# Optimization experiments

Hardware: AMD Instinct MI355X
Metric: run time of the kernel (lower is better)

## Reference

```python
import jax, jax.numpy as jnp
import numpy as np

D_IN = 2048
H1 = D_IN // 4      # 512
H2 = D_IN // 16     # 128
N_EXP = 8
N_CLS = 10
BATCH = 16384


def setup_inputs() -> dict:
    key = jax.random.key(0)
    ks = jax.random.split(key, 16)
    s = lambda k, shape, fan_in: jax.random.normal(k, shape, jnp.float32) / np.sqrt(fan_in)
    return {
        "fs": jax.random.normal(ks[0], (BATCH, D_IN // 2), jnp.float32),
        "fp": jax.random.normal(ks[1], (BATCH, D_IN // 2), jnp.float32),
        # gate MLP params (output = num_source, softmax)
        "gW1": s(ks[2], (D_IN, H1), D_IN), "gb1": jnp.zeros((H1,), jnp.float32),
        "gW2": s(ks[3], (H1, H2), H1),     "gb2": jnp.zeros((H2,), jnp.float32),
        "gW3": s(ks[4], (H2, N_EXP), H2), "gb3": jnp.zeros((N_EXP,), jnp.float32),
        # stacked expert MLP params (output = num classes, log_softmax)
        "eW1": s(ks[5], (N_EXP, D_IN, H1), D_IN), "eb1": jnp.zeros((N_EXP, H1), jnp.float32),
        "eW2": s(ks[6], (N_EXP, H1, H2), H1),     "eb2": jnp.zeros((N_EXP, H2), jnp.float32),
        "eW3": s(ks[7], (N_EXP, H2, N_CLS), H2),  "eb3": jnp.zeros((N_EXP, N_CLS), jnp.float32),
    }


def reference(fs, fp, gW1, gb1, gW2, gb2, gW3, gb3, eW1, eb1, eW2, eb2, eW3, eb3):
    features = jnp.concatenate([fs, fp], axis=-1)            # [B, D_IN]

    # Gate MLP on detached features (detach is a no-op for fwd), softmax output
    g = jax.nn.relu(features @ gW1 + gb1)
    g = jax.nn.relu(g @ gW2 + gb2)
    gate_outs = jax.nn.softmax(g @ gW3 + gb3, axis=-1)       # [B, E]

    # All experts as batched GEMMs over stacked weights, log_softmax output
    h = jax.nn.relu(jnp.einsum('bd,edh->beh', features, eW1) + eb1[None])   # [B, E, H1]
    h = jax.nn.relu(jnp.einsum('beh,ehk->bek', h, eW2) + eb2[None])         # [B, E, H2]
    logits = jnp.einsum('bek,eko->beo', h, eW3) + eb3[None]                 # [B, E, C]
    expert_outs = jax.nn.log_softmax(logits, axis=-1)                       # [B, E, C]

    # Gate-weighted sum over experts
    output = jnp.einsum('be,bec->bc', gate_outs, expert_outs)               # [B, C]
    return output, gate_outs
```

## Files before the change

### kernel.cpp

```cpp
#include <hip/hip_runtime.h>
#include <hip/hip_bf16.h>

#define B_SZ   16384
#define DIN    2048
#define H1_SZ  512
#define H2_SZ  128
#define N_EXP  8
#define N_CLS  10
#define N1     4608
#define N2     1152

typedef __attribute__((ext_vector_type(8))) __bf16 bf16x8;
typedef __attribute__((ext_vector_type(4))) float  floatx4;
typedef __attribute__((ext_vector_type(4))) short  short4v;
typedef __attribute__((ext_vector_type(8))) short  short8v;

__device__ __forceinline__ float bf2f(short s) {
  unsigned int u = ((unsigned int)(unsigned short)s) << 16;
  float f; __builtin_memcpy(&f, &u, 4); return f;
}

__global__ void convert_features_kernel(const float* __restrict__ fs,
                                        const float* __restrict__ fp,
                                        __hip_bfloat16* __restrict__ X) {
  const int nf8 = B_SZ * (DIN / 8);
  const float4* fs4 = (const float4*)fs;
  const float4* fp4 = (const float4*)fp;
  for (int i = blockIdx.x * blockDim.x + threadIdx.x; i < nf8;
       i += gridDim.x * blockDim.x) {
    int c = i & 255;
    int row = i >> 8;
    float4 v0, v1;
    if (c < 128) {
      v0 = fs4[(size_t)row * 256 + 2 * c];
      v1 = fs4[(size_t)row * 256 + 2 * c + 1];
    } else {
      int cc = c - 128;
      v0 = fp4[(size_t)row * 256 + 2 * cc];
      v1 = fp4[(size_t)row * 256 + 2 * cc + 1];
    }
    union { short8v v8; __hip_bfloat16 h[8]; } u;
    u.h[0] = __float2bfloat16(v0.x);
    u.h[1] = __float2bfloat16(v0.y);
    u.h[2] = __float2bfloat16(v0.z);
    u.h[3] = __float2bfloat16(v0.w);
    u.h[4] = __float2bfloat16(v1.x);
    u.h[5] = __float2bfloat16(v1.y);
    u.h[6] = __float2bfloat16(v1.z);
    u.h[7] = __float2bfloat16(v1.w);
    *(short8v*)(X + (size_t)i * 8) = u.v8;
  }
}

__global__ void transpose_convert_kernel(const float* __restrict__ expert_src,
                                         const float* __restrict__ gate_src,
                                         int K, int H, int E,
                                         __hip_bfloat16* __restrict__ out) {
  __shared__ float t[32][33];
  int k0 = blockIdx.x * 32;
  int n0 = blockIdx.y * 32;
  int e = n0 / H;
  const float* src; int h0;
  if (e < E) { src = expert_src + (size_t)e * K * H; h0 = n0 - e * H; }
  else       { src = gate_src;                       h0 = n0 - E * H; }
  int tx = threadIdx.x, ty = threadIdx.y;
  #pragma unroll
  for (int j = 0; j < 4; ++j) {
    int r = ty + j * 8;
    t[r][tx] = src[(size_t)(k0 + r) * H + h0 + tx];
  }
  __syncthreads();
  #pragma unroll
  for (int j = 0; j < 4; ++j) {
    int r = ty + j * 8;
    out[(size_t)(n0 + r) * K + k0 + tx] = __float2bfloat16(t[tx][r]);
  }
}

template <bool NT>
__device__ __forceinline__ void gemm_core(
    const __hip_bfloat16* __restrict__ A,  int lda,
    const __hip_bfloat16* __restrict__ BT, int K,
    const float* __restrict__ bias,
    __hip_bfloat16* __restrict__ O, int ldo) {
  __shared__ __align__(16) __hip_bfloat16 As[128 * 64];
  __shared__ __align__(16) __hip_bfloat16 Bs[128 * 64];

  const int tid  = threadIdx.x;
  const int lane = tid & 63;
  const int wave = tid >> 6;
  const int wm   = (wave >> 1) * 64;
  const int wn   = (wave & 1) * 64;
  const int lrow  = lane & 15;
  const int lquad = lane >> 4;

  floatx4 acc[4][4] = {};

  for (int k0 = 0; k0 < K; k0 += 64) {
    #pragma unroll
    for (int j = 0; j < 4; ++j) {
      int chunk = j * 256 + tid;
      int mi = chunk >> 3;
      int cs = chunk & 7;
      int cl = cs ^ (mi & 7);
      __builtin_amdgcn_global_load_lds(
          (const __attribute__((address_space(1))) unsigned int*)(A + (size_t)mi * lda + k0 + cl * 8),
          (__attribute__((address_space(3))) unsigned int*)(As + chunk * 8),
          16, 0, 0);
      __builtin_amdgcn_global_load_lds(
          (const __attribute__((address_space(1))) unsigned int*)(BT + (size_t)mi * K + k0 + cl * 8),
          (__attribute__((address_space(3))) unsigned int*)(Bs + chunk * 8),
          16, 0, 0);
    }
    __syncthreads();
    #pragma unroll
    for (int ks = 0; ks < 2; ++ks) {
      bf16x8 a[4], b[4];
      #pragma unroll
      for (int t = 0; t < 4; ++t) {
        int ar = wm + t * 16 + lrow;
        int br = wn + t * 16 + lrow;
        int ca = (ks * 4 + lquad) ^ (ar & 7);
        int cb = (ks * 4 + lquad) ^ (br & 7);
        a[t] = *(const bf16x8*)(As + ar * 64 + ca * 8);
        b[t] = *(const bf16x8*)(Bs + br * 64 + cb * 8);
      }
      #pragma unroll
      for (int mt = 0; mt < 4; ++mt)
        #pragma unroll
        for (int nt = 0; nt < 4; ++nt)
          acc[mt][nt] = __builtin_amdgcn_mfma_f32_16x16x32_bf16(
              a[mt], b[nt], acc[mt][nt], 0, 0, 0);
    }
    __syncthreads();
  }

  #pragma unroll
  for (int nt = 0; nt < 4; ++nt) {
    int col = wn + nt * 16 + lrow;
    float bv = bias[col];
    #pragma unroll
    for (int mt = 0; mt < 4; ++mt) {
      #pragma unroll
      for (int r = 0; r < 4; ++r) {
        int row = wm + mt * 16 + lquad * 4 + r;
        float v = acc[mt][nt][r] + bv;
        v = v > 0.f ? v : 0.f;
        __hip_bfloat16 hv = __float2bfloat16(v);
        if (NT) {
          __builtin_nontemporal_store(
              *reinterpret_cast<unsigned short*>(&hv),
              reinterpret_cast<unsigned short*>(&O[(size_t)row * ldo + col]));
        } else {
          O[(size_t)row * ldo + col] = hv;
        }
      }
    }
  }
}

__global__ __launch_bounds__(256, 2) void gemm1_kernel(
    const __hip_bfloat16* __restrict__ X, const __hip_bfloat16* __restrict__ W1T,
    const float* __restrict__ eb1, const float* __restrict__ gb1,
    __hip_bfloat16* __restrict__ H1) {
  int flat = blockIdx.x;
  int swz  = (flat & 7) * 576 + (flat >> 3);
  int m0 = (swz / 36) * 128;
  int n0 = (swz % 36) * 128;
  const float* bias = (n0 < N_EXP * H1_SZ) ? (eb1 + n0) : (gb1 + (n0 - N_EXP * H1_SZ));
  gemm_core<true>(X + (size_t)m0 * DIN, DIN,
                  W1T + (size_t)n0 * DIN, DIN,
                  bias,
                  H1 + (size_t)m0 * N1 + n0, N1);
}

__global__ __launch_bounds__(256, 2) void gemm2_kernel(
    const __hip_bfloat16* __restrict__ H1, const __hip_bfloat16* __restrict__ W2T,
    const float* __restrict__ eb2, const float* __restrict__ gb2,
    __hip_bfloat16* __restrict__ H2) {
  int m0 = blockIdx.y * 128;
  int z  = blockIdx.z;
  const float* bias = (z < N_EXP) ? (eb2 + z * H2_SZ) : gb2;
  gemm_core<false>(H1 + (size_t)m0 * N1 + z * H1_SZ, N1,
                   W2T + (size_t)z * H2_SZ * H1_SZ, H1_SZ,
                   bias,
                   H2 + (size_t)m0 * N2 + z * H2_SZ, N2);
}

__global__ __launch_bounds__(256) void layer3_kernel(
    const __hip_bfloat16* __restrict__ H2,
    const float* __restrict__ gW3, const float* __restrict__ gb3,
    const float* __restrict__ eW3, const float* __restrict__ eb3,
    float* __restrict__ out, float* __restrict__ gate_out) {
  int tid  = threadIdx.x;
  int j    = tid & 7;
  int rloc = tid >> 3;
  long row = (long)blockIdx.x * 32 + rloc;
  const __hip_bfloat16* hrow = H2 + row * N2;

  float accg = 0.f;
  float acc[N_CLS];
  #pragma unroll
  for (int c = 0; c < N_CLS; ++c) acc[c] = 0.f;

  #pragma unroll 4
  for (int k8 = 0; k8 < 16; ++k8) {
    short8v hg8 = *(const short8v*)(hrow + N_EXP * H2_SZ + k8 * 8);
    short8v he8 = *(const short8v*)(hrow + j * H2_SZ + k8 * 8);
    #pragma unroll
    for (int t = 0; t < 8; ++t) {
      int k = k8 * 8 + t;
      float hg = bf2f(hg8[t]);
      float he = bf2f(he8[t]);
      accg += hg * gW3[k * N_EXP + j];
      const float* w = eW3 + (size_t)(j * H2_SZ + k) * N_CLS;
      #pragma unroll
      for (int c = 0; c < N_CLS; ++c) acc[c] += he * w[c];
    }
  }

  float gj = accg + gb3[j];
  float mx = gj;
  mx = fmaxf(mx, __shfl_xor(mx, 1));
  mx = fmaxf(mx, __shfl_xor(mx, 2));
  mx = fmaxf(mx, __shfl_xor(mx, 4));
  float ex = __expf(gj - mx);
  float s = ex;
  s += __shfl_xor(s, 1);
  s += __shfl_xor(s, 2);
  s += __shfl_xor(s, 4);
  float gp = ex / s;

  float lg[N_CLS];
  float lm = -1e30f;
  #pragma unroll
  for (int c = 0; c < N_CLS; ++c) {
    lg[c] = acc[c] + eb3[j * N_CLS + c];
    lm = fmaxf(lm, lg[c]);
  }
  float es = 0.f;
  #pragma unroll
  for (int c = 0; c < N_CLS; ++c) es += __expf(lg[c] - lm);
  float lse = lm + __logf(es);

  float o[N_CLS];
  #pragma unroll
  for (int c = 0; c < N_CLS; ++c) o[c] = gp * (lg[c] - lse);
  #pragma unroll
  for (int c = 0; c < N_CLS; ++c) {
    o[c] += __shfl_xor(o[c], 1);
    o[c] += __shfl_xor(o[c], 2);
    o[c] += __shfl_xor(o[c], 4);
  }

  gate_out[row * N_EXP + j] = gp;
  if (j == 0) {
    #pragma unroll
    for (int c = 0; c < N_CLS; ++c) out[row * N_CLS + c] = o[c];
  }
}

extern "C" void kernel_launch(void* const* d_in, const int* in_sizes, int n_in,
                              void* d_out, int out_size, void* d_ws, size_t ws_size,
                              hipStream_t stream) {
  const float* fs  = (const float*)d_in[0];
  const float* fp  = (const float*)d_in[1];
  const float* gW1 = (const float*)d_in[2];
  const float* gb1 = (const float*)d_in[3];
  const float* gW2 = (const float*)d_in[4];
  const float* gb2 = (const float*)d_in[5];
  const float* gW3 = (const float*)d_in[6];
  const float* gb3 = (const float*)d_in[7];
  const float* eW1 = (const float*)d_in[8];
  const float* eb1 = (const float*)d_in[9];
  const float* eW2 = (const float*)d_in[10];
  const float* eb2 = (const float*)d_in[11];
  const float* eW3 = (const float*)d_in[12];
  const float* eb3 = (const float*)d_in[13];
  float* out = (float*)d_out;

  char* ws = (char*)d_ws;
  __hip_bfloat16* X   = (__hip_bfloat16*)ws;
  __hip_bfloat16* H2  = X;
  __hip_bfloat16* W1T = (__hip_bfloat16*)(ws + 67108864);
  __hip_bfloat16* W2T = (__hip_bfloat16*)(ws + 85983232);
  __hip_bfloat16* H1  = (__hip_bfloat16*)(ws + 87162880);

  convert_features_kernel<<<2048, 256, 0, stream>>>(fs, fp, X);
  transpose_convert_kernel<<<dim3(DIN / 32, N1 / 32), dim3(32, 8), 0, stream>>>(
      eW1, gW1, DIN, H1_SZ, N_EXP, W1T);
  transpose_convert_kernel<<<dim3(H1_SZ / 32, N2 / 32), dim3(32, 8), 0, stream>>>(
      eW2, gW2, H1_SZ, H2_SZ, N_EXP, W2T);
  gemm1_kernel<<<4608, 256, 0, stream>>>(X, W1T, eb1, gb1, H1);
  gemm2_kernel<<<dim3(1, B_SZ / 128, N_EXP + 1), 256, 0, stream>>>(H1, W2T, eb2, gb2, H2);
  layer3_kernel<<<B_SZ / 32, 256, 0, stream>>>(H2, gW3, gb3, eW3, eb3,
                                               out, out + (size_t)B_SZ * N_CLS);
}
```

Before: 707.1 us.

## Merge prep kernels into one launch and drop gemm1 swizzle and nontemporal stores

The feature conversion and the two weight transpose kernels are merged into a single prep kernel that dispatches on block index, removing two launches and letting the three jobs overlap. Gemm1 goes back from an XCD-style swizzled 1D grid to a plain 2D grid. Its H1 output is now written with regular stores instead of nontemporal ones. Together these cut launch overhead but may lose the L2 locality the swizzle gave and the cache behaviour of the nontemporal stores.

Result: faster. 614.4 us (median of 2 runs) (-13.1%).

```diff
diff --git a/kernel.cpp b/kernel.cpp
--- a/kernel.cpp
+++ b/kernel.cpp
@@ -20,50 +20,20 @@
   float f; __builtin_memcpy(&f, &u, 4); return f;
 }
 
-__global__ void convert_features_kernel(const float* __restrict__ fs,
-                                        const float* __restrict__ fp,
-                                        __hip_bfloat16* __restrict__ X) {
-  const int nf8 = B_SZ * (DIN / 8);
-  const float4* fs4 = (const float4*)fs;
-  const float4* fp4 = (const float4*)fp;
-  for (int i = blockIdx.x * blockDim.x + threadIdx.x; i < nf8;
-       i += gridDim.x * blockDim.x) {
-    int c = i & 255;
-    int row = i >> 8;
-    float4 v0, v1;
-    if (c < 128) {
-      v0 = fs4[(size_t)row * 256 + 2 * c];
-      v1 = fs4[(size_t)row * 256 + 2 * c + 1];
-    } else {
-      int cc = c - 128;
-      v0 = fp4[(size_t)row * 256 + 2 * cc];
-      v1 = fp4[(size_t)row * 256 + 2 * cc + 1];
-    }
-    union { short8v v8; __hip_bfloat16 h[8]; } u;
-    u.h[0] = __float2bfloat16(v0.x);
-    u.h[1] = __float2bfloat16(v0.y);
-    u.h[2] = __float2bfloat16(v0.z);
-    u.h[3] = __float2bfloat16(v0.w);
-    u.h[4] = __float2bfloat16(v1.x);
-    u.h[5] = __float2bfloat16(v1.y);
-    u.h[6] = __float2bfloat16(v1.z);
-    u.h[7] = __float2bfloat16(v1.w);
-    *(short8v*)(X + (size_t)i * 8) = u.v8;
-  }
-}
-
-__global__ void transpose_convert_kernel(const float* __restrict__ expert_src,
-                                         const float* __restrict__ gate_src,
-                                         int K, int H, int E,
-                                         __hip_bfloat16* __restrict__ out) {
-  __shared__ float t[32][33];
-  int k0 = blockIdx.x * 32;
-  int n0 = blockIdx.y * 32;
+#define CONV_BLOCKS 2048
+#define T1_BLOCKS   (64 * 144)
+#define T2_BLOCKS   (16 * 36)
+#define PREP_BLOCKS (CONV_BLOCKS + T1_BLOCKS + T2_BLOCKS)
+
+__device__ __forceinline__ void transpose_tile(
+    const float* __restrict__ expert_src, const float* __restrict__ gate_src,
+    int K, int H, int E, __hip_bfloat16* __restrict__ out,
+    int k0, int n0, int tid, float (*t)[33]) {
   int e = n0 / H;
   const float* src; int h0;
   if (e < E) { src = expert_src + (size_t)e * K * H; h0 = n0 - e * H; }
   else       { src = gate_src;                       h0 = n0 - E * H; }
-  int tx = threadIdx.x, ty = threadIdx.y;
+  int tx = tid & 31, ty = tid >> 5;
   #pragma unroll
   for (int j = 0; j < 4; ++j) {
     int r = ty + j * 8;
@@ -77,7 +47,57 @@
   }
 }
 
-template <bool NT>
+__global__ __launch_bounds__(256) void prep_kernel(
+    const float* __restrict__ fs, const float* __restrict__ fp,
+    __hip_bfloat16* __restrict__ X,
+    const float* __restrict__ eW1, const float* __restrict__ gW1,
+    __hip_bfloat16* __restrict__ W1T,
+    const float* __restrict__ eW2, const float* __restrict__ gW2,
+    __hip_bfloat16* __restrict__ W2T) {
+  __shared__ float t[32][33];
+  int bid = blockIdx.x;
+  int tid = threadIdx.x;
+
+  if (bid < CONV_BLOCKS) {
+    const int nf8 = B_SZ * (DIN / 8);
+    const float4* fs4 = (const float4*)fs;
+    const float4* fp4 = (const float4*)fp;
+    for (int i = bid * 256 + tid; i < nf8; i += CONV_BLOCKS * 256) {
+      int c = i & 255;
+      int row = i >> 8;
+      float4 v0, v1;
+      if (c < 128) {
+        v0 = fs4[(size_t)row * 256 + 2 * c];
+        v1 = fs4[(size_t)row * 256 + 2 * c + 1];
+      } else {
+        int cc = c - 128;
+        v0 = fp4[(size_t)row * 256 + 2 * cc];
+        v1 = fp4[(size_t)row * 256 + 2 * cc + 1];
+      }
+      union { short8v v8; __hip_bfloat16 h[8]; } u;
+      u.h[0] = __float2bfloat16(v0.x);
+      u.h[1] = __float2bfloat16(v0.y);
+      u.h[2] = __float2bfloat16(v0.z);
+      u.h[3] = __float2bfloat16(v0.w);
+      u.h[4] = __float2bfloat16(v1.x);
+      u.h[5] = __float2bfloat16(v1.y);
+      u.h[6] = __float2bfloat16(v1.z);
+      u.h[7] = __float2bfloat16(v1.w);
+      *(short8v*)(X + (size_t)i * 8) = u.v8;
+    }
+  } else if (bid < CONV_BLOCKS + T1_BLOCKS) {
+    int bz = bid - CONV_BLOCKS;
+    int k0 = (bz & 63) * 32;
+    int n0 = (bz >> 6) * 32;
+    transpose_tile(eW1, gW1, DIN, H1_SZ, N_EXP, W1T, k0, n0, tid, t);
+  } else {
+    int bz = bid - CONV_BLOCKS - T1_BLOCKS;
+    int k0 = (bz & 15) * 32;
+    int n0 = (bz >> 4) * 32;
+    transpose_tile(eW2, gW2, H1_SZ, H2_SZ, N_EXP, W2T, k0, n0, tid, t);
+  }
+}
+
 __device__ __forceinline__ void gemm_core(
     const __hip_bfloat16* __restrict__ A,  int lda,
     const __hip_bfloat16* __restrict__ BT, int K,
@@ -146,14 +166,7 @@
         int row = wm + mt * 16 + lquad * 4 + r;
         float v = acc[mt][nt][r] + bv;
         v = v > 0.f ? v : 0.f;
-        __hip_bfloat16 hv = __float2bfloat16(v);
-        if (NT) {
-          __builtin_nontemporal_store(
-              *reinterpret_cast<unsigned short*>(&hv),
-              reinterpret_cast<unsigned short*>(&O[(size_t)row * ldo + col]));
-        } else {
-          O[(size_t)row * ldo + col] = hv;
-        }
+        O[(size_t)row * ldo + col] = __float2bfloat16(v);
       }
     }
   }
@@ -163,15 +176,13 @@
     const __hip_bfloat16* __restrict__ X, const __hip_bfloat16* __restrict__ W1T,
     const float* __restrict__ eb1, const float* __restrict__ gb1,
     __hip_bfloat16* __restrict__ H1) {
-  int flat = blockIdx.x;
-  int swz  = (flat & 7) * 576 + (flat >> 3);
-  int m0 = (swz / 36) * 128;
-  int n0 = (swz % 36) * 128;
+  int m0 = blockIdx.y * 128;
+  int n0 = blockIdx.x * 128;
   const float* bias = (n0 < N_EXP * H1_SZ) ? (eb1 + n0) : (gb1 + (n0 - N_EXP * H1_SZ));
-  gemm_core<true>(X + (size_t)m0 * DIN, DIN,
-                  W1T + (size_t)n0 * DIN, DIN,
-                  bias,
-                  H1 + (size_t)m0 * N1 + n0, N1);
+  gemm_core(X + (size_t)m0 * DIN, DIN,
+            W1T + (size_t)n0 * DIN, DIN,
+            bias,
+            H1 + (size_t)m0 * N1 + n0, N1);
 }
 
 __global__ __launch_bounds__(256, 2) void gemm2_kernel(
@@ -181,10 +192,10 @@
   int m0 = blockIdx.y * 128;
   int z  = blockIdx.z;
   const float* bias = (z < N_EXP) ? (eb2 + z * H2_SZ) : gb2;
-  gemm_core<false>(H1 + (size_t)m0 * N1 + z * H1_SZ, N1,
-                   W2T + (size_t)z * H2_SZ * H1_SZ, H1_SZ,
-                   bias,
-                   H2 + (size_t)m0 * N2 + z * H2_SZ, N2);
+  gemm_core(H1 + (size_t)m0 * N1 + z * H1_SZ, N1,
+            W2T + (size_t)z * H2_SZ * H1_SZ, H1_SZ,
+            bias,
+            H2 + (size_t)m0 * N2 + z * H2_SZ, N2);
 }
 
 __global__ __launch_bounds__(256) void layer3_kernel(
@@ -286,12 +297,10 @@
   __hip_bfloat16* W2T = (__hip_bfloat16*)(ws + 85983232);
   __hip_bfloat16* H1  = (__hip_bfloat16*)(ws + 87162880);
 
-  convert_features_kernel<<<2048, 256, 0, stream>>>(fs, fp, X);
-  transpose_convert_kernel<<<dim3(DIN / 32, N1 / 32), dim3(32, 8), 0, stream>>>(
-      eW1, gW1, DIN, H1_SZ, N_EXP, W1T);
-  transpose_convert_kernel<<<dim3(H1_SZ / 32, N2 / 32), dim3(32, 8), 0, stream>>>(
-      eW2, gW2, H1_SZ, H2_SZ, N_EXP, W2T);
-  gemm1_kernel<<<4608, 256, 0, stream>>>(X, W1T, eb1, gb1, H1);
+  prep_kernel<<<PREP_BLOCKS, 256, 0, stream>>>(fs, fp, X,
+                                               eW1, gW1, W1T,
+                                               eW2, gW2, W2T);
+  gemm1_kernel<<<dim3(N1 / 128, B_SZ / 128), 256, 0, stream>>>(X, W1T, eb1, gb1, H1);
   gemm2_kernel<<<dim3(1, B_SZ / 128, N_EXP + 1), 256, 0, stream>>>(H1, W2T, eb2, gb2, H2);
   layer3_kernel<<<B_SZ / 32, 256, 0, stream>>>(H2, gW3, gb3, eW3, eb3,
                                                out, out + (size_t)B_SZ * N_CLS);
```
